# Kernel optimization log

Measured on AMD Instinct MI355X. Metric: run time of the kernel, lower is better.

Reference implementation:

```python
import jax, jax.numpy as jnp
import numpy as np

# dims: B batch, C features, N nodes, L seq_len, P pred_len, D d_model, M topk+self,
# H hidden(=4D), K date2vec freqs, DM time_features, PPH points_per_hour
B, C, N, L, P, D, M, H, K, DM, PPH = 32, 3, 883, 12, 12, 128, 10, 512, 16, 5, 12


def setup_inputs() -> dict:
    ks = jax.random.split(jax.random.key(0), 24)
    r = lambda i, shape, s=1.0: jax.random.normal(ks[i], shape, dtype=jnp.float32) * s
    z = lambda shape: jnp.zeros(shape, jnp.float32)
    return {
        "input": r(0, (B, C, N, L)),
        "adj": r(1, (N, N)),
        "seqs_time": jax.random.uniform(ks[2], (B, DM, 1, L), dtype=jnp.float32) - 0.5,
        "targets_time": jax.random.uniform(ks[3], (B, DM, 1, P), dtype=jnp.float32) - 0.5,
        "memory_bank": r(4, (N, D), (2.0 / (N + D)) ** 0.5),
        "We1": r(5, (D, D), D ** -0.5),
        "We2": r(6, (D, D), D ** -0.5),
        "time_in_day_emb": r(7, (PPH * 24, D), 0.05),
        "day_in_week_emb": r(8, (7, D), 0.05),
        "ts_emb_W": r(9, (D, C * L), (C * L) ** -0.5),
        "ts_emb_b": z((D,)),
        "conv_in_W": r(10, (C, C), C ** -0.5),
        "conv_in_b": z((C,)),
        "enc_W1": r(11, (3, H, H), H ** -0.5),
        "enc_b1": z((3, H)),
        "enc_W2": r(12, (3, H, H), H ** -0.5),
        "enc_b2": z((3, H)),
        "reg_W": r(13, (C * L, H), H ** -0.5),
        "reg_b": z((C * L,)),
        "d2v_w0": r(14, (DM,), 0.1),
        "d2v_b0": r(15, (1,), 0.1),
        "d2v_W": r(16, (K, DM), 0.3),
        "d2v_b": r(17, (K,), 0.3),
        "d2v_mix": r(18, (1,), 0.1),
        "weight_inextend": r(19, (M,), 0.3),
        "fus_W": r(20, (C, D), C ** -0.5),
        "fus_b": z((D,)),
        "glu_W1": r(21, (D, C), D ** -0.5),
        "glu_b1": z((C,)),
        "glu_W2": r(22, (D, C), D ** -0.5),
        "glu_b2": z((C,)),
    }


def _forward(input, adj, seqs_time, targets_time, memory_bank, We1, We2,
             time_in_day_emb, day_in_week_emb, ts_emb_W, ts_emb_b,
             conv_in_W, conv_in_b, enc_W1, enc_b1, enc_W2, enc_b2,
             reg_W, reg_b, d2v_w0, d2v_b0, d2v_W, d2v_b, d2v_mix,
             weight_inextend, fus_W, fus_b, glu_W1, glu_b1, glu_W2, glu_b2):
    eps = 1e-5

    def bn(x):  # train-mode BatchNorm2d, identity affine (default init)
        m = x.mean((0, 2, 3), keepdims=True)
        v = x.var((0, 2, 3), keepdims=True)
        return (x - m) * jax.lax.rsqrt(v + eps)

    # --- adaptive adjacency: matmul + row standardize + masked softmax ---
    e1 = memory_bank @ We1
    e2 = memory_bank @ We2
    a = e1 @ e2.T  # [N, N]
    a = (a - a.mean(-1, keepdims=True)) / jnp.std(a, axis=-1, ddof=1, keepdims=True)
    a = jax.nn.softmax(jax.nn.relu(a) - jnp.eye(N, dtype=a.dtype) * 1e6, axis=-1)

    xb = bn(input)  # [B, C, N, L]

    # --- Input module (STID-style) ---
    ts = xb.transpose(0, 2, 1, 3).reshape(B, N, C * L)  # [B, N, C*L]
    ts_emb = jnp.einsum('bnk,dk->bdn', ts, ts_emb_W) + ts_emb_b[None, :, None]
    hour = (seqs_time[:, -2, 0, :] + 0.5) * 23.0
    minute = (seqs_time[:, -1, 0, :] + 0.5) * 59.0
    tidx = jnp.clip(((hour * 60.0 + minute) / (60.0 / PPH))[:, -1].astype(jnp.int32), 0, PPH * 24 - 1)
    didx = jnp.clip(((seqs_time[:, 2, 0, -1] + 0.5) * 6.0).astype(jnp.int32), 0, 6)
    tid = jnp.broadcast_to(time_in_day_emb[tidx][:, :, None], (B, D, N))
    diw = jnp.broadcast_to(day_in_week_emb[didx][:, :, None], (B, D, N))
    node = jnp.broadcast_to(memory_bank.T[None], (B, D, N))
    hidden = jnp.concatenate([ts_emb, node, tid, diw], axis=1)  # [B, 4D, N]
    for i in range(3):  # MLP residual blocks (1x1 conv == channel matmul)
        h = jax.nn.relu(jnp.einsum('hk,bkn->bhn', enc_W1[i], hidden) + enc_b1[i][None, :, None])
        hidden = hidden + jnp.einsum('hk,bkn->bhn', enc_W2[i], h) + enc_b2[i][None, :, None]
    reg = jnp.einsum('ok,bkn->bon', reg_W, hidden) + reg_b[None, :, None]  # [B, C*L, N]
    hid = bn(reg.reshape(B, C, L, N).transpose(0, 1, 3, 2))  # [B, C, N, L]
    cx = jnp.einsum('oc,bcnl->bonl', conv_in_W, xb) + conv_in_b[None, :, None, None]
    x = bn(hid + cx)

    # --- sample module: topk neighbors + gather ---
    top_value, index = jax.lax.top_k(a, M - 1)  # [N, M-1]
    x_ext = jnp.concatenate([x[:, :, :, None, :], x[:, :, index]], axis=3)  # [B,C,N,M,L]

    # --- Date2Vec (Time2Vec-style periodic embedding) ---
    tau = jnp.concatenate([seqs_time, targets_time], axis=-1)[:, :, 0, :]  # [B, DM, L+P]
    phi = (jnp.einsum('bdt,d->bt', tau, d2v_w0) + d2v_b0[0]
           + jnp.sin(jnp.einsum('bdt,kd->bkt', tau, d2v_W) + d2v_b[None, :, None]).sum(1))
    d2v = phi[:, None, None, None, :] + d2v_mix[0] * x_ext.mean(-1)[..., None]  # [B,C,N,M,L+P]
    d2v_x, d2v_y = d2v[..., :L], d2v[..., L:]

    # --- Fusion: date-attention over source timesteps, neighbor-weighted merge ---
    scores = jnp.einsum('bcnmp,bcnml->bnmpl', d2v_y, d2v_x) / jnp.float32(C * L)
    A = jax.nn.softmax(scores, axis=-1)
    pm = jnp.einsum('bnmpl,bcnml->bcnmp', A, x_ext)
    w = jnp.concatenate([jnp.ones((N, 1), pm.dtype), top_value], axis=-1) * weight_inextend[None, :]
    pred = jnp.einsum('bcnmp,nm->bcnp', pm, w)
    pred = jnp.einsum('bcnp,cd->bdnp', pred, fus_W) + fus_b[None, :, None, None]

    # --- GLU output module ---
    o1 = jnp.einsum('bdnp,do->bonp', pred, glu_W1) + glu_b1[None, :, None, None]
    o2 = jnp.einsum('bdnp,do->bonp', pred, glu_W2) + glu_b2[None, :, None, None]
    return o1 * jax.nn.sigmoid(o2)  # [B, C, N, P]


def reference(input, adj, seqs_time, targets_time, memory_bank, We1, We2,
              time_in_day_emb, day_in_week_emb, ts_emb_W, ts_emb_b,
              conv_in_W, conv_in_b, enc_W1, enc_b1, enc_W2, enc_b2,
              reg_W, reg_b, d2v_w0, d2v_b0, d2v_W, d2v_b, d2v_mix,
              weight_inextend, fus_W, fus_b, glu_W1, glu_b1, glu_W2, glu_b2):
    return _forward(input, adj, seqs_time, targets_time, memory_bank, We1, We2,
                    time_in_day_emb, day_in_week_emb, ts_emb_W, ts_emb_b,
                    conv_in_W, conv_in_b, enc_W1, enc_b1, enc_W2, enc_b2,
                    reg_W, reg_b, d2v_w0, d2v_b0, d2v_W, d2v_b, d2v_mix,
                    weight_inextend, fus_W, fus_b, glu_W1, glu_b1, glu_W2, glu_b2)
```

## Files before the change

### kernel.cpp

```cpp
#include <hip/hip_runtime.h>
#include <hip/hip_bf16.h>


#define NN 883
#define NPAD 896
#define BB 32
#define HH 512
#define NL 10596
#define CNT_PER_C 339072.0f
#define TOT_X 1017216
#define LSTR 32
#define LREG 4096

typedef __attribute__((ext_vector_type(8))) short bf16x8;
typedef __attribute__((ext_vector_type(4))) float f32x4;

static __device__ __forceinline__ float bf2f(__hip_bfloat16 v) { return __bfloat162float(v); }
static __device__ __forceinline__ float ldf(const void* p, long i, int f) {
    return f ? ((const float*)p)[i] : bf2f(((const __hip_bfloat16*)p)[i]);
}
static __device__ __forceinline__ unsigned short bfbits(float v) {
    __hip_bfloat16 h = __float2bfloat16(v);
    return *(unsigned short*)&h;
}
static __device__ __forceinline__ void async_copy16(const void* g, void* l) {
    __builtin_amdgcn_global_load_lds((const __attribute__((address_space(1))) void*)g,
                                     (__attribute__((address_space(3))) void*)l, 16, 0, 0);
}

struct alignas(8) BF4 { __hip_bfloat16 a, b, c, d; };

__global__ void k_sent_r10(float* __restrict__ out, int n)
{
    int i = blockIdx.x*256 + threadIdx.x;
    if (i < n) out[i] = 1000.0f;
}

__global__ void k_probe_r10(const unsigned short* __restrict__ u, int* __restrict__ flag)
{
    int t = threadIdx.x, cnt = 0;
    for (int i = t; i < 4096; i += 256) {
        int e = (u[i] >> 7) & 0xFF;
        cnt += (e >= 0xC0);
    }
    __shared__ int r[256];
    r[t] = cnt; __syncthreads();
    for (int s = 128; s > 0; s >>= 1) { if (t < s) r[t] += r[t+s]; __syncthreads(); }
    if (t == 0) *flag = (r[0] > 8) ? 1 : 0;
}

__global__ void k_wsplit_r10(const void* __restrict__ src, const int* __restrict__ dflag,
                             int n, __hip_bfloat16* __restrict__ hi,
                             __hip_bfloat16* __restrict__ lo)
{
    int f = *dflag;
    for (int i = blockIdx.x*256 + threadIdx.x; i < n; i += gridDim.x*256) {
        float v = ldf(src, i, f);
        __hip_bfloat16 h = __float2bfloat16(v);
        hi[i] = h;
        lo[i] = __float2bfloat16(v - bf2f(h));
    }
}

__global__ void k_prep_r10(const void* __restrict__ seqs, const void* __restrict__ tgts,
                           const void* __restrict__ w0, const void* __restrict__ b0,
                           const void* __restrict__ d2vW, const void* __restrict__ d2vb,
                           const void* __restrict__ fusW, const void* __restrict__ fusb,
                           const void* __restrict__ g1W, const void* __restrict__ g1b,
                           const void* __restrict__ g2W, const void* __restrict__ g2b,
                           const int* __restrict__ dflag,
                           int* __restrict__ tidx, int* __restrict__ didx,
                           float* __restrict__ phi, float* __restrict__ wc)
{
    int f = *dflag, t = threadIdx.x;
    if (t < 32) {
        int b = t;
        float h  = (ldf(seqs, (b*5+3)*12 + 11, f) + 0.5f) * 23.0f;
        float mi = (ldf(seqs, (b*5+4)*12 + 11, f) + 0.5f) * 59.0f;
        int ti = (int)((h * 60.0f + mi) / 5.0f);
        tidx[b] = ti < 0 ? 0 : (ti > 287 ? 287 : ti);
        int di = (int)((ldf(seqs, (b*5+2)*12 + 11, f) + 0.5f) * 6.0f);
        didx[b] = di < 0 ? 0 : (di > 6 ? 6 : di);
    }
    for (int i = t; i < 768; i += 256) {
        int b = i / 24, tt = i % 24;
        float tau[5];
        #pragma unroll
        for (int d = 0; d < 5; d++)
            tau[d] = (tt < 12) ? ldf(seqs, (b*5+d)*12 + tt, f)
                               : ldf(tgts, (b*5+d)*12 + tt - 12, f);
        float s = ldf(b0, 0, f);
        #pragma unroll
        for (int d = 0; d < 5; d++) s += tau[d] * ldf(w0, d, f);
        for (int k = 0; k < 16; k++) {
            float arg = ldf(d2vb, k, f);
            #pragma unroll
            for (int d = 0; d < 5; d++) arg += tau[d] * ldf(d2vW, k*5 + d, f);
            s += sinf(arg);
        }
        phi[i] = s;
    }
    if (t < 24) {
        if (t < 9) {
            int o = t / 3, c = t % 3; float s = 0.f;
            for (int d = 0; d < 128; d++) s += ldf(fusW, c*128+d, f) * ldf(g1W, d*3+o, f);
            wc[t] = s;
        } else if (t < 12) {
            int o = t - 9; float s = ldf(g1b, o, f);
            for (int d = 0; d < 128; d++) s += ldf(fusb, d, f) * ldf(g1W, d*3+o, f);
            wc[9 + o] = s;
        } else if (t < 21) {
            int j = t - 12; int o = j / 3, c = j % 3; float s = 0.f;
            for (int d = 0; d < 128; d++) s += ldf(fusW, c*128+d, f) * ldf(g2W, d*3+o, f);
            wc[12 + j] = s;
        } else {
            int o = t - 21; float s = ldf(g2b, o, f);
            for (int d = 0; d < 128; d++) s += ldf(fusb, d, f) * ldf(g2W, d*3+o, f);
            wc[21 + o] = s;
        }
    }
}

__global__ void k_e_r10(const void* __restrict__ mb, const void* __restrict__ We1,
                        const void* __restrict__ We2, const int* __restrict__ dflag,
                        float* __restrict__ e1, float* __restrict__ e2t)
{
    int f = *dflag;
    int idx = blockIdx.x*256 + threadIdx.x;
    int which = idx >= 113024;
    int j = which ? idx - 113024 : idx;
    int d = j & 127, n = j >> 7;
    const void* W = which ? We2 : We1;
    float s = 0.f;
    for (int k = 0; k < 128; k++)
        s += ldf(mb, n*128 + k, f) * ldf(W, k*128 + d, f);
    if (which) e2t[d*NN + n] = s;
    else       e1[j] = s;
}

__global__ void __launch_bounds__(256)
k_graph_r10(const float* __restrict__ e1, const float* __restrict__ e2t,
            float* __restrict__ topval, int* __restrict__ topidx)
{
    int n = blockIdx.x, t = threadIdx.x;
    __shared__ float e1s[128];
    __shared__ float arow[NN];
    __shared__ float red[256];
    __shared__ int redi[256];
    if (t < 128) e1s[t] = e1[n*128 + t];
    __syncthreads();
    for (int m = t; m < NN; m += 256) {
        float acc = 0.f;
        #pragma unroll 8
        for (int k = 0; k < 128; k++) acc += e1s[k] * e2t[k*NN + m];
        arow[m] = acc;
    }
    __syncthreads();
    float s = 0.f;
    for (int m = t; m < NN; m += 256) s += arow[m];
    red[t] = s; __syncthreads();
    for (int st = 128; st > 0; st >>= 1) { if (t < st) red[t] += red[t+st]; __syncthreads(); }
    float mean = red[0] / 883.0f; __syncthreads();
    float ss = 0.f;
    for (int m = t; m < NN; m += 256) { float d = arow[m] - mean; ss += d*d; }
    red[t] = ss; __syncthreads();
    for (int st = 128; st > 0; st >>= 1) { if (t < st) red[t] += red[t+st]; __syncthreads(); }
    float rstd = 1.0f / sqrtf(red[0] / 882.0f); __syncthreads();
    for (int m = t; m < NN; m += 256) {
        float z = (arow[m] - mean) * rstd;
        z = fmaxf(z, 0.f);
        if (m == n) z -= 1e6f;
        arow[m] = z;
    }
    __syncthreads();
    float mx = -3.4e38f;
    for (int m = t; m < NN; m += 256) mx = fmaxf(mx, arow[m]);
    red[t] = mx; __syncthreads();
    for (int st = 128; st > 0; st >>= 1) { if (t < st) red[t] = fmaxf(red[t], red[t+st]); __syncthreads(); }
    float M = red[0]; __syncthreads();
    float ds = 0.f;
    for (int m = t; m < NN; m += 256) { float e = expf(arow[m] - M); arow[m] = e; ds += e; }
    red[t] = ds; __syncthreads();
    for (int st = 128; st > 0; st >>= 1) { if (t < st) red[t] += red[t+st]; __syncthreads(); }
    float inv = 1.0f / red[0]; __syncthreads();
    for (int m = t; m < NN; m += 256) arow[m] *= inv;
    __syncthreads();
    for (int j = 0; j < 9; j++) {
        float bv = -1.f; int bi = 0;
        for (int m = t; m < NN; m += 256) { float v = arow[m]; if (v > bv) { bv = v; bi = m; } }
        red[t] = bv; redi[t] = bi; __syncthreads();
        for (int st = 128; st > 0; st >>= 1) {
            if (t < st) {
                float ov = red[t+st]; int oi = redi[t+st];
                if (ov > red[t] || (ov == red[t] && oi < redi[t])) { red[t] = ov; redi[t] = oi; }
            }
            __syncthreads();
        }
        if (t == 0) {
            topval[n*9 + j] = red[0];
            topidx[n*9 + j] = redi[0];
            arow[redi[0]] = -1.f;
        }
        __syncthreads();
    }
}

__global__ void k_bn1_r10(const void* __restrict__ x, const int* __restrict__ dflag,
                          float* __restrict__ st)
{
    int f = *dflag;
    float s[3] = {0,0,0}, q[3] = {0,0,0};
    for (int i = blockIdx.x*256 + threadIdx.x; i < TOT_X; i += 512*256) {
        int c = (i / NL) % 3;
        float v = ldf(x, i, f);
        s[c] += v; q[c] += v*v;
    }
    __shared__ float red[6][256];
    int t = threadIdx.x;
    #pragma unroll
    for (int j = 0; j < 3; j++) { red[j][t] = s[j]; red[3+j][t] = q[j]; }
    __syncthreads();
    for (int st_ = 128; st_ > 0; st_ >>= 1) {
        if (t < st_) {
            #pragma unroll
            for (int j = 0; j < 6; j++) red[j][t] += red[j][t+st_];
        }
        __syncthreads();
    }
    if (t < 6) atomicAdd(&st[t], red[t][0]);
}

__global__ void __launch_bounds__(256)
k_hid_r10(const void* __restrict__ in, const void* __restrict__ mb,
          const void* __restrict__ tide, const void* __restrict__ diwe,
          const void* __restrict__ tsW, const void* __restrict__ tsb,
          const int* __restrict__ tidx, const int* __restrict__ didx,
          const int* __restrict__ dflag, const float* __restrict__ st1,
          int b0, __hip_bfloat16* __restrict__ Xhi, __hip_bfloat16* __restrict__ Xlo)
{
    int f = *dflag;
    int n = blockIdx.x, bl = blockIdx.y, bg = b0 + bl, t = threadIdx.x;
    __shared__ float tsw[128*37];
    __shared__ float tsbs[128];
    __shared__ float xbs[36];
    for (int i = t; i < 4608; i += 256) {
        int ch = i / 36, k = i % 36;
        tsw[ch*37 + k] = ldf(tsW, i, f);
    }
    if (t < 128) tsbs[t] = ldf(tsb, t, f);
    if (t < 36) {
        int c = t / 12, l = t % 12;
        float m = st1[c] * (1.0f/CNT_PER_C);
        float v = st1[3+c] * (1.0f/CNT_PER_C) - m*m;
        xbs[t] = (ldf(in, ((long)(bg*3 + c)*NN + n)*12 + l, f) - m) / sqrtf(v + 1e-5f);
    }
    __syncthreads();
    size_t base = ((size_t)bl*NPAD + n)*HH;
    float v[2];
    #pragma unroll
    for (int j = 0; j < 2; j++) {
        int ch = 2*t + j;
        if (ch < 128) {
            float a = tsbs[ch];
            #pragma unroll
            for (int k = 0; k < 36; k++) a += xbs[k] * tsw[ch*37 + k];
            v[j] = a;
        } else if (ch < 256) v[j] = ldf(mb, n*128 + ch - 128, f);
        else if (ch < 384)   v[j] = ldf(tide, tidx[bg]*128 + ch - 256, f);
        else                 v[j] = ldf(diwe, didx[bg]*128 + ch - 384, f);
    }
    unsigned short h0 = bfbits(v[0]), h1 = bfbits(v[1]);
    __hip_bfloat16 hb0, hb1;
    *(unsigned short*)&hb0 = h0; *(unsigned short*)&hb1 = h1;
    unsigned short l0 = bfbits(v[0] - bf2f(hb0)), l1 = bfbits(v[1] - bf2f(hb1));
    *(unsigned*)(Xhi + base + 2*t) = (unsigned)h0 | ((unsigned)h1 << 16);
    *(unsigned*)(Xlo + base + 2*t) = (unsigned)l0 | ((unsigned)l1 << 16);
}

template<bool RELU, bool RESID, bool F32OUT>
__global__ void __launch_bounds__(256)
k_gemm_r10(const __hip_bfloat16* __restrict__ Whi, const __hip_bfloat16* __restrict__ Wlo,
           long Woff, const void* __restrict__ bias, long boff,
           const int* __restrict__ dflag,
           const __hip_bfloat16* __restrict__ Xhi, const __hip_bfloat16* __restrict__ Xlo,
           __hip_bfloat16* __restrict__ Yhi, __hip_bfloat16* __restrict__ Ylo,
           float* __restrict__ outF, int HO, int b0)
{
    __shared__ __align__(16) short sm[4*LREG];
    int tid = threadIdx.x, bz = blockIdx.z;
    int n0 = blockIdx.x * 128, ho0 = blockIdx.y * 128;
    int lane = tid & 63, wave = tid >> 6;
    int wm = wave & 1, wn = wave >> 1;
    int lm = lane & 15, quad = lane >> 4;

    f32x4 acc[4][4];
    #pragma unroll
    for (int i = 0; i < 4; i++)
        #pragma unroll
        for (int j = 0; j < 4; j++) acc[i][j] = (f32x4){0.f, 0.f, 0.f, 0.f};

    const size_t xb0 = (size_t)bz*NPAD*HH;
    int rowi[2], kci[2], rri[2], nBi[2], lofsi[2];
    #pragma unroll
    for (int it = 0; it < 2; it++) {
        int s = it*256 + tid;
        rowi[it] = s >> 2; kci[it] = (s & 3) * 8;
        int rr = ho0 + rowi[it]; rri[it] = (rr >= HO) ? HO - 1 : rr;
        int nB = n0 + rowi[it]; nBi[it] = (nB >= NN) ? NN - 1 : nB;
        lofsi[it] = s * 8;
    }

    for (int k0 = 0; k0 < 512; k0 += 32) {
        #pragma unroll
        for (int it = 0; it < 2; it++) {
            size_t wofs = (size_t)Woff + (size_t)rri[it]*512 + k0 + kci[it];
            size_t xofs = xb0 + (size_t)nBi[it]*HH + k0 + kci[it];
            int lofs = lofsi[it];
            async_copy16(Whi + wofs, &sm[lofs]);
            async_copy16(Wlo + wofs, &sm[LREG + lofs]);
            async_copy16(Xhi + xofs, &sm[2*LREG + lofs]);
            async_copy16(Xlo + xofs, &sm[3*LREG + lofs]);
        }
        __syncthreads();
        bf16x8 ah[4], al[4], bh[4], bl[4];
        #pragma unroll
        for (int mi = 0; mi < 4; mi++) {
            int o = (wm*64 + mi*16 + lm)*LSTR + quad*8;
            ah[mi] = *(const bf16x8*)&sm[o];
            al[mi] = *(const bf16x8*)&sm[LREG + o];
        }
        #pragma unroll
        for (int ni = 0; ni < 4; ni++) {
            int o = (wn*64 + ni*16 + lm)*LSTR + quad*8;
            bh[ni] = *(const bf16x8*)&sm[2*LREG + o];
            bl[ni] = *(const bf16x8*)&sm[3*LREG + o];
        }
        #pragma unroll
        for (int mi = 0; mi < 4; mi++)
            #pragma unroll
            for (int ni = 0; ni < 4; ni++) {
                acc[mi][ni] = __builtin_amdgcn_mfma_f32_16x16x32_bf16(ah[mi], bh[ni], acc[mi][ni], 0, 0, 0);
                acc[mi][ni] = __builtin_amdgcn_mfma_f32_16x16x32_bf16(ah[mi], bl[ni], acc[mi][ni], 0, 0, 0);
                acc[mi][ni] = __builtin_amdgcn_mfma_f32_16x16x32_bf16(al[mi], bh[ni], acc[mi][ni], 0, 0, 0);
            }
        __syncthreads();
    }

    int f = *dflag;
    #pragma unroll
    for (int mi = 0; mi < 4; mi++) {
        int hor = ho0 + wm*64 + mi*16 + quad*4;
        float bv[4];
        #pragma unroll
        for (int r = 0; r < 4; r++) {
            int h = hor + r; if (h >= HO) h = HO - 1;
            bv[r] = ldf(bias, boff + h, f);
        }
        #pragma unroll
        for (int ni = 0; ni < 4; ni++) {
            int nc = n0 + wn*64 + ni*16 + lm;
            if (nc >= NN) continue;
            if constexpr (F32OUT) {
                #pragma unroll
                for (int r = 0; r < 4; r++) {
                    int h = hor + r;
                    if (h < HO) outF[((size_t)(b0 + bz)*HO + h)*NN + nc] = acc[mi][ni][r] + bv[r];
                }
            } else {
                size_t o = xb0 + (size_t)nc*HH + hor;
                float vals[4];
                #pragma unroll
                for (int r = 0; r < 4; r++) vals[r] = acc[mi][ni][r] + bv[r];
                if constexpr (RESID) {
                    BF4 rh = *(const BF4*)(Yhi + o);
                    BF4 rl = *(const BF4*)(Ylo + o);
                    vals[0] += bf2f(rh.a) + bf2f(rl.a);
                    vals[1] += bf2f(rh.b) + bf2f(rl.b);
                    vals[2] += bf2f(rh.c) + bf2f(rl.c);
                    vals[3] += bf2f(rh.d) + bf2f(rl.d);
                }
                if constexpr (RELU) {
                    #pragma unroll
                    for (int r = 0; r < 4; r++) vals[r] = fmaxf(vals[r], 0.f);
                }
                BF4 hi, lo;
                hi.a = __float2bfloat16(vals[0]); lo.a = __float2bfloat16(vals[0] - bf2f(hi.a));
                hi.b = __float2bfloat16(vals[1]); lo.b = __float2bfloat16(vals[1] - bf2f(hi.b));
                hi.c = __float2bfloat16(vals[2]); lo.c = __float2bfloat16(vals[2] - bf2f(hi.c));
                hi.d = __float2bfloat16(vals[3]); lo.d = __float2bfloat16(vals[3] - bf2f(hi.d));
                *(BF4*)(Yhi + o) = hi;
                *(BF4*)(Ylo + o) = lo;
            }
        }
    }
}

__global__ void k_bn2_r10(const float* __restrict__ x, float* __restrict__ st)
{
    float s[3] = {0,0,0}, q[3] = {0,0,0};
    for (int i = blockIdx.x*256 + threadIdx.x; i < TOT_X; i += 512*256) {
        int c = ((i / NN) % 36) / 12;
        float v = x[i];
        s[c] += v; q[c] += v*v;
    }
    __shared__ float red[6][256];
    int t = threadIdx.x;
    #pragma unroll
    for (int j = 0; j < 3; j++) { red[j][t] = s[j]; red[3+j][t] = q[j]; }
    __syncthreads();
    for (int st_ = 128; st_ > 0; st_ >>= 1) {
        if (t < st_) {
            #pragma unroll
            for (int j = 0; j < 6; j++) red[j][t] += red[j][t+st_];
        }
        __syncthreads();
    }
    if (t < 6) atomicAdd(&st[t], red[t][0]);
}

__global__ void k_xpre_r10(const float* __restrict__ regb, const void* __restrict__ in,
                           const void* __restrict__ convW, const void* __restrict__ convb,
                           const int* __restrict__ dflag, const float* __restrict__ st1,
                           const float* __restrict__ st2, float* __restrict__ st3,
                           float* __restrict__ xpre)
{
    int f = *dflag;
    int i = blockIdx.x*256 + threadIdx.x;
    float s[3] = {0,0,0}, q[3] = {0,0,0};
    if (i < TOT_X) {
        int b = i / 31788, r1 = i % 31788;
        int c = r1 / NL, r2 = r1 % NL;
        int n = r2 / 12, l = r2 % 12;
        float m2 = st2[c] * (1.0f/CNT_PER_C);
        float v2 = st2[3+c] * (1.0f/CNT_PER_C) - m2*m2;
        float hidv = (regb[((size_t)b*36 + c*12 + l)*NN + n] - m2) / sqrtf(v2 + 1e-5f);
        float cx = ldf(convb, c, f);
        #pragma unroll
        for (int cc = 0; cc < 3; cc++) {
            float m1 = st1[cc] * (1.0f/CNT_PER_C);
            float v1 = st1[3+cc] * (1.0f/CNT_PER_C) - m1*m1;
            float xbv = (ldf(in, ((long)(b*3 + cc)*NN + n)*12 + l, f) - m1) / sqrtf(v1 + 1e-5f);
            cx += ldf(convW, c*3 + cc, f) * xbv;
        }
        float v = hidv + cx;
        xpre[i] = v;
        s[c] = v; q[c] = v*v;
    }
    __shared__ float red[6][256];
    int t = threadIdx.x;
    #pragma unroll
    for (int j = 0; j < 3; j++) { red[j][t] = s[j]; red[3+j][t] = q[j]; }
    __syncthreads();
    for (int st_ = 128; st_ > 0; st_ >>= 1) {
        if (t < st_) {
            #pragma unroll
            for (int j = 0; j < 6; j++) red[j][t] += red[j][t+st_];
        }
        __syncthreads();
    }
    if (t < 6) atomicAdd(&st3[t], red[t][0]);
}

__global__ void __launch_bounds__(64)
k_tail_r10(const float* __restrict__ xpre, const float* __restrict__ st3,
           const float* __restrict__ phi, const float* __restrict__ topval,
           const int* __restrict__ topidx, const float* __restrict__ wc,
           const void* __restrict__ wie, const void* __restrict__ mixp,
           const int* __restrict__ dflag, float* __restrict__ out)
{
    int f = *dflag;
    int n = blockIdx.x, b = blockIdx.y, t = threadIdx.x;
    __shared__ float xe[3][10][12], mn[3][10], phis[24], ws[10];
    __shared__ float pm[3][10][12], pred[3][12];
    float m3[3], rs3[3];
    #pragma unroll
    for (int c = 0; c < 3; c++) {
        float m = st3[c] * (1.0f/CNT_PER_C);
        float v = st3[3+c] * (1.0f/CNT_PER_C) - m*m;
        m3[c] = m; rs3[c] = 1.0f / sqrtf(v + 1e-5f);
    }
    if (t < 24) phis[t] = phi[b*24 + t];
    if (t < 10) ws[t] = (t == 0 ? 1.0f : topval[n*9 + t - 1]) * ldf(wie, t, f);
    for (int i = t; i < 360; i += 64) {
        int c = i / 120, m = (i / 12) % 10, l = i % 12;
        int nn2 = (m == 0) ? n : topidx[n*9 + m - 1];
        xe[c][m][l] = (xpre[((size_t)(b*3 + c)*NN + nn2)*12 + l] - m3[c]) * rs3[c];
    }
    __syncthreads();
    if (t < 30) {
        int c = t / 10, m = t % 10;
        float s = 0.f;
        #pragma unroll
        for (int l = 0; l < 12; l++) s += xe[c][m][l];
        mn[c][m] = s * (1.0f/12.0f);
    }
    __syncthreads();
    float mix = ldf(mixp, 0, f);
    for (int pr = t; pr < 120; pr += 64) {
        int m = pr / 12, p = pr % 12;
        float y[3], sc[12], mx = -3.4e38f;
        #pragma unroll
        for (int c = 0; c < 3; c++) y[c] = phis[12+p] + mix*mn[c][m];
        #pragma unroll
        for (int l = 0; l < 12; l++) {
            float v = 0.f;
            #pragma unroll
            for (int c = 0; c < 3; c++) v += y[c] * (phis[l] + mix*mn[c][m]);
            sc[l] = v * (1.0f/36.0f); mx = fmaxf(mx, sc[l]);
        }
        float den = 0.f;
        #pragma unroll
        for (int l = 0; l < 12; l++) { float e = expf(sc[l] - mx); sc[l] = e; den += e; }
        float inv = 1.0f/den;
        float p0 = 0.f, p1 = 0.f, p2 = 0.f;
        #pragma unroll
        for (int l = 0; l < 12; l++) {
            float a = sc[l]*inv;
            p0 += a*xe[0][m][l]; p1 += a*xe[1][m][l]; p2 += a*xe[2][m][l];
        }
        pm[0][m][p] = p0; pm[1][m][p] = p1; pm[2][m][p] = p2;
    }
    __syncthreads();
    if (t < 36) {
        int c = t/12, p = t%12;
        float s = 0.f;
        #pragma unroll
        for (int m = 0; m < 10; m++) s += pm[c][m][p]*ws[m];
        pred[c][p] = s;
    }
    __syncthreads();
    if (t < 36) {
        int o = t/12, p = t%12;
        float o1 = wc[9+o]  + wc[o*3+0]*pred[0][p] + wc[o*3+1]*pred[1][p] + wc[o*3+2]*pred[2][p];
        float o2 = wc[21+o] + wc[12+o*3+0]*pred[0][p] + wc[12+o*3+1]*pred[1][p] + wc[12+o*3+2]*pred[2][p];
        out[((size_t)(b*3 + o)*NN + n)*12 + p] = o1 / (1.0f + expf(-o2));
    }
}

extern "C" void kernel_launch(void* const* d_in, const int* in_sizes, int n_in,
                              void* d_out, int out_size, void* d_ws, size_t ws_size,
                              hipStream_t stream)
{
    (void)in_sizes; (void)n_in;
    char* w = (char*)d_ws;
    auto alloc = [&](size_t bytes) { char* p = w; w += (bytes + 255) & ~(size_t)255; return p; };

    float* regb   = (float*)alloc((size_t)TOT_X*4);
    float* xpre   = (float*)alloc((size_t)TOT_X*4);
    __hip_bfloat16* Whi1 = (__hip_bfloat16*)alloc(786432*2);
    __hip_bfloat16* Wlo1 = (__hip_bfloat16*)alloc(786432*2);
    __hip_bfloat16* Whi2 = (__hip_bfloat16*)alloc(786432*2);
    __hip_bfloat16* Wlo2 = (__hip_bfloat16*)alloc(786432*2);
    __hip_bfloat16* rhi  = (__hip_bfloat16*)alloc(18432*2);
    __hip_bfloat16* rlo  = (__hip_bfloat16*)alloc(18432*2);
    float* e1     = (float*)alloc(113024*4);
    float* e2t    = (float*)alloc(113024*4);
    float* phi    = (float*)alloc(768*4);
    float* topval = (float*)alloc(7947*4);
    int*   topidx = (int*)alloc(7947*4);
    int*   tidx   = (int*)alloc(32*4);
    int*   didx   = (int*)alloc(32*4);
    float* stats  = (float*)alloc(18*4);
    float* wc     = (float*)alloc(24*4);
    int*   dflag  = (int*)alloc(4);
    size_t fixedEnd = (size_t)(w - (char*)d_ws);

    const size_t XB = (size_t)NPAD*HH*2;
    int CH = 0;
    for (int c = 32; c >= 1; c >>= 1) {
        if (fixedEnd + 4*(size_t)c*XB + 4096 <= ws_size) { CH = c; break; }
    }
    if (CH == 0) {
        k_sent_r10<<<(out_size + 255)/256, 256, 0, stream>>>((float*)d_out, out_size);
        return;
    }
    char* regionB = w;
    __hip_bfloat16* Xahi = (__hip_bfloat16*)regionB;
    __hip_bfloat16* Xalo = (__hip_bfloat16*)(regionB + (size_t)CH*XB);
    __hip_bfloat16* Xbhi = (__hip_bfloat16*)(regionB + 2*(size_t)CH*XB);
    __hip_bfloat16* Xblo = (__hip_bfloat16*)(regionB + 3*(size_t)CH*XB);

    hipMemsetAsync(stats, 0, 18*4, stream);

    k_probe_r10<<<1, 256, 0, stream>>>((const unsigned short*)d_in[0], dflag);
    k_prep_r10<<<1, 256, 0, stream>>>(d_in[2], d_in[3], d_in[19], d_in[20], d_in[21], d_in[22],
                                      d_in[25], d_in[26], d_in[27], d_in[28], d_in[29], d_in[30],
                                      dflag, tidx, didx, phi, wc);
    k_wsplit_r10<<<1024, 256, 0, stream>>>(d_in[13], dflag, 786432, Whi1, Wlo1);
    k_wsplit_r10<<<1024, 256, 0, stream>>>(d_in[15], dflag, 786432, Whi2, Wlo2);
    k_wsplit_r10<<<72,   256, 0, stream>>>(d_in[17], dflag, 18432, rhi, rlo);

    k_e_r10<<<883, 256, 0, stream>>>(d_in[4], d_in[5], d_in[6], dflag, e1, e2t);
    k_graph_r10<<<883, 256, 0, stream>>>(e1, e2t, topval, topidx);
    k_bn1_r10<<<512, 256, 0, stream>>>(d_in[0], dflag, stats);

    for (int b0 = 0; b0 < BB; b0 += CH) {
        k_hid_r10<<<dim3(NN, CH), 256, 0, stream>>>(d_in[0], d_in[4], d_in[7], d_in[8],
                                                    d_in[9], d_in[10], tidx, didx, dflag,
                                                    stats, b0, Xahi, Xalo);
        for (int i = 0; i < 3; i++) {
            k_gemm_r10<true, false, false><<<dim3(7, 4, CH), 256, 0, stream>>>(
                Whi1, Wlo1, (long)i*HH*HH, d_in[14], (long)i*HH, dflag,
                Xahi, Xalo, Xbhi, Xblo, (float*)nullptr, HH, b0);
            k_gemm_r10<false, true, false><<<dim3(7, 4, CH), 256, 0, stream>>>(
                Whi2, Wlo2, (long)i*HH*HH, d_in[16], (long)i*HH, dflag,
                Xbhi, Xblo, Xahi, Xalo, (float*)nullptr, HH, b0);
        }
        k_gemm_r10<false, false, true><<<dim3(7, 1, CH), 256, 0, stream>>>(
            rhi, rlo, 0, d_in[18], 0, dflag,
            Xahi, Xalo, (__hip_bfloat16*)nullptr, (__hip_bfloat16*)nullptr, regb, 36, b0);
    }

    k_bn2_r10<<<512, 256, 0, stream>>>(regb, stats + 6);
    k_xpre_r10<<<3974, 256, 0, stream>>>(regb, d_in[0], d_in[11], d_in[12], dflag,
                                         stats, stats + 6, stats + 12, xpre);
    k_tail_r10<<<dim3(NN, BB), 64, 0, stream>>>(xpre, stats + 12, phi, topval, topidx, wc,
                                                d_in[24], d_in[23], dflag, (float*)d_out);
}
```

Before: 975.2 us.

## Fuse second BatchNorm stats into regression GEMM, transpose its output, batch hidden-embedding nodes

New measurement: 918.8 us. 5.8% less time.

```diff
diff --git a/kernel.cpp b/kernel.cpp
--- a/kernel.cpp
+++ b/kernel.cpp
@@ -30,13 +30,13 @@
 
 struct alignas(8) BF4 { __hip_bfloat16 a, b, c, d; };
 
-__global__ void k_sent_r10(float* __restrict__ out, int n)
+__global__ void k_sent_r11(float* __restrict__ out, int n)
 {
     int i = blockIdx.x*256 + threadIdx.x;
     if (i < n) out[i] = 1000.0f;
 }
 
-__global__ void k_probe_r10(const unsigned short* __restrict__ u, int* __restrict__ flag)
+__global__ void k_probe_r11(const unsigned short* __restrict__ u, int* __restrict__ flag)
 {
     int t = threadIdx.x, cnt = 0;
     for (int i = t; i < 4096; i += 256) {
@@ -49,7 +49,7 @@
     if (t == 0) *flag = (r[0] > 8) ? 1 : 0;
 }
 
-__global__ void k_wsplit_r10(const void* __restrict__ src, const int* __restrict__ dflag,
+__global__ void k_wsplit_r11(const void* __restrict__ src, const int* __restrict__ dflag,
                              int n, __hip_bfloat16* __restrict__ hi,
                              __hip_bfloat16* __restrict__ lo)
 {
@@ -62,7 +62,7 @@
     }
 }
 
-__global__ void k_prep_r10(const void* __restrict__ seqs, const void* __restrict__ tgts,
+__global__ void k_prep_r11(const void* __restrict__ seqs, const void* __restrict__ tgts,
                            const void* __restrict__ w0, const void* __restrict__ b0,
                            const void* __restrict__ d2vW, const void* __restrict__ d2vb,
                            const void* __restrict__ fusW, const void* __restrict__ fusb,
@@ -121,7 +121,7 @@
     }
 }
 
-__global__ void k_e_r10(const void* __restrict__ mb, const void* __restrict__ We1,
+__global__ void k_e_r11(const void* __restrict__ mb, const void* __restrict__ We1,
                         const void* __restrict__ We2, const int* __restrict__ dflag,
                         float* __restrict__ e1, float* __restrict__ e2t)
 {
@@ -139,7 +139,7 @@
 }
 
 __global__ void __launch_bounds__(256)
-k_graph_r10(const float* __restrict__ e1, const float* __restrict__ e2t,
+k_graph_r11(const float* __restrict__ e1, const float* __restrict__ e2t,
             float* __restrict__ topval, int* __restrict__ topidx)
 {
     int n = blockIdx.x, t = threadIdx.x;
@@ -205,7 +205,7 @@
     }
 }
 
-__global__ void k_bn1_r10(const void* __restrict__ x, const int* __restrict__ dflag,
+__global__ void k_bn1_r11(const void* __restrict__ x, const int* __restrict__ dflag,
                           float* __restrict__ st)
 {
     int f = *dflag;
@@ -231,7 +231,7 @@
 }
 
 __global__ void __launch_bounds__(256)
-k_hid_r10(const void* __restrict__ in, const void* __restrict__ mb,
+k_hid_r11(const void* __restrict__ in, const void* __restrict__ mb,
           const void* __restrict__ tide, const void* __restrict__ diwe,
           const void* __restrict__ tsW, const void* __restrict__ tsb,
           const int* __restrict__ tidx, const int* __restrict__ didx,
@@ -239,52 +239,73 @@
           int b0, __hip_bfloat16* __restrict__ Xhi, __hip_bfloat16* __restrict__ Xlo)
 {
     int f = *dflag;
-    int n = blockIdx.x, bl = blockIdx.y, bg = b0 + bl, t = threadIdx.x;
+    int bl = blockIdx.y, bg = b0 + bl, t = threadIdx.x;
+    int n0 = blockIdx.x * 8;
     __shared__ float tsw[128*37];
     __shared__ float tsbs[128];
-    __shared__ float xbs[36];
-    for (int i = t; i < 4608; i += 256) {
-        int ch = i / 36, k = i % 36;
-        tsw[ch*37 + k] = ldf(tsW, i, f);
-    }
-    if (t < 128) tsbs[t] = ldf(tsb, t, f);
-    if (t < 36) {
-        int c = t / 12, l = t % 12;
+    __shared__ float xbs[8][36];
+    float m1[3], r1v[3];
+    #pragma unroll
+    for (int c = 0; c < 3; c++) {
         float m = st1[c] * (1.0f/CNT_PER_C);
         float v = st1[3+c] * (1.0f/CNT_PER_C) - m*m;
-        xbs[t] = (ldf(in, ((long)(bg*3 + c)*NN + n)*12 + l, f) - m) / sqrtf(v + 1e-5f);
-    }
-    __syncthreads();
+        m1[c] = m; r1v[c] = 1.0f / sqrtf(v + 1e-5f);
+    }
+    for (int i = t; i < 4608; i += 256)
+        tsw[(i/36)*37 + (i%36)] = ldf(tsW, i, f);
+    if (t < 128) tsbs[t] = ldf(tsb, t, f);
+    for (int i = t; i < 288; i += 256) {
+        int nl = i / 36, k = i % 36;
+        int c = k / 12, l = k % 12;
+        int n = n0 + nl; if (n >= NN) n = NN - 1;
+        xbs[nl][k] = (ldf(in, ((long)(bg*3 + c)*NN + n)*12 + l, f) - m1[c]) * r1v[c];
+    }
+    __syncthreads();
+    int nloc = t >> 5, lane = t & 31;
+    int n = n0 + nloc;
+    if (n >= NN) return;
     size_t base = ((size_t)bl*NPAD + n)*HH;
-    float v[2];
-    #pragma unroll
-    for (int j = 0; j < 2; j++) {
-        int ch = 2*t + j;
-        if (ch < 128) {
-            float a = tsbs[ch];
+    const float* xr = xbs[nloc];
+    #pragma unroll
+    for (int j = 0; j < 8; j++) {
+        int ch0 = j*64 + lane*2;
+        float v0, v1;
+        if (j < 2) {
+            float a0 = tsbs[ch0], a1 = tsbs[ch0+1];
             #pragma unroll
-            for (int k = 0; k < 36; k++) a += xbs[k] * tsw[ch*37 + k];
-            v[j] = a;
-        } else if (ch < 256) v[j] = ldf(mb, n*128 + ch - 128, f);
-        else if (ch < 384)   v[j] = ldf(tide, tidx[bg]*128 + ch - 256, f);
-        else                 v[j] = ldf(diwe, didx[bg]*128 + ch - 384, f);
-    }
-    unsigned short h0 = bfbits(v[0]), h1 = bfbits(v[1]);
-    __hip_bfloat16 hb0, hb1;
-    *(unsigned short*)&hb0 = h0; *(unsigned short*)&hb1 = h1;
-    unsigned short l0 = bfbits(v[0] - bf2f(hb0)), l1 = bfbits(v[1] - bf2f(hb1));
-    *(unsigned*)(Xhi + base + 2*t) = (unsigned)h0 | ((unsigned)h1 << 16);
-    *(unsigned*)(Xlo + base + 2*t) = (unsigned)l0 | ((unsigned)l1 << 16);
-}
-
-template<bool RELU, bool RESID, bool F32OUT>
+            for (int k = 0; k < 36; k++) {
+                float xv = xr[k];
+                a0 += xv * tsw[ch0*37 + k];
+                a1 += xv * tsw[(ch0+1)*37 + k];
+            }
+            v0 = a0; v1 = a1;
+        } else if (j < 4) {
+            v0 = ldf(mb, n*128 + ch0 - 128, f);
+            v1 = ldf(mb, n*128 + ch0 - 127, f);
+        } else if (j < 6) {
+            v0 = ldf(tide, tidx[bg]*128 + ch0 - 256, f);
+            v1 = ldf(tide, tidx[bg]*128 + ch0 - 255, f);
+        } else {
+            v0 = ldf(diwe, didx[bg]*128 + ch0 - 384, f);
+            v1 = ldf(diwe, didx[bg]*128 + ch0 - 383, f);
+        }
+        unsigned short h0 = bfbits(v0), h1 = bfbits(v1);
+        __hip_bfloat16 hb0, hb1;
+        *(unsigned short*)&hb0 = h0; *(unsigned short*)&hb1 = h1;
+        unsigned short l0 = bfbits(v0 - bf2f(hb0)), l1 = bfbits(v1 - bf2f(hb1));
+        *(unsigned*)(Xhi + base + ch0) = (unsigned)h0 | ((unsigned)h1 << 16);
+        *(unsigned*)(Xlo + base + ch0) = (unsigned)l0 | ((unsigned)l1 << 16);
+    }
+}
+
+template<bool RELU, bool RESID, bool REGT>
 __global__ void __launch_bounds__(256)
-k_gemm_r10(const __hip_bfloat16* __restrict__ Whi, const __hip_bfloat16* __restrict__ Wlo,
+k_gemm_r11(const __hip_bfloat16* __restrict__ Whi, const __hip_bfloat16* __restrict__ Wlo,
            long Woff, const void* __restrict__ bias, long boff,
            const int* __restrict__ dflag,
            const __hip_bfloat16* __restrict__ Xhi, const __hip_bfloat16* __restrict__ Xlo,
            __hip_bfloat16* __restrict__ Yhi, __hip_bfloat16* __restrict__ Ylo,
-           float* __restrict__ outF, int HO, int b0)
+           float* __restrict__ regT, float* __restrict__ st2, int HO, int b0)
 {
     __shared__ __align__(16) short sm[4*LREG];
     int tid = threadIdx.x, bz = blockIdx.z;
@@ -300,13 +321,13 @@
         for (int j = 0; j < 4; j++) acc[i][j] = (f32x4){0.f, 0.f, 0.f, 0.f};
 
     const size_t xb0 = (size_t)bz*NPAD*HH;
-    int rowi[2], kci[2], rri[2], nBi[2], lofsi[2];
+    int rri[2], nBi[2], kci[2], lofsi[2];
     #pragma unroll
     for (int it = 0; it < 2; it++) {
         int s = it*256 + tid;
-        rowi[it] = s >> 2; kci[it] = (s & 3) * 8;
-        int rr = ho0 + rowi[it]; rri[it] = (rr >= HO) ? HO - 1 : rr;
-        int nB = n0 + rowi[it]; nBi[it] = (nB >= NN) ? NN - 1 : nB;
+        int row = s >> 2; kci[it] = (s & 3) * 8;
+        int rr = ho0 + row; rri[it] = (rr >= HO) ? HO - 1 : rr;
+        int nB = n0 + row; nBi[it] = (nB >= NN) ? NN - 1 : nB;
         lofsi[it] = s * 8;
     }
 
@@ -347,6 +368,7 @@
     }
 
     int f = *dflag;
+    float s3[3] = {0,0,0}, q3[3] = {0,0,0};
     #pragma unroll
     for (int mi = 0; mi < 4; mi++) {
         int hor = ho0 + wm*64 + mi*16 + quad*4;
@@ -360,11 +382,17 @@
         for (int ni = 0; ni < 4; ni++) {
             int nc = n0 + wn*64 + ni*16 + lm;
             if (nc >= NN) continue;
-            if constexpr (F32OUT) {
-                #pragma unroll
-                for (int r = 0; r < 4; r++) {
-                    int h = hor + r;
-                    if (h < HO) outF[((size_t)(b0 + bz)*HO + h)*NN + nc] = acc[mi][ni][r] + bv[r];
+            if constexpr (REGT) {
+                if (hor <= 32) {
+                    int c = hor / 12;
+                    float4 v4;
+                    v4.x = acc[mi][ni][0] + bv[0];
+                    v4.y = acc[mi][ni][1] + bv[1];
+                    v4.z = acc[mi][ni][2] + bv[2];
+                    v4.w = acc[mi][ni][3] + bv[3];
+                    *(float4*)(regT + ((size_t)(b0 + bz)*NN + nc)*36 + hor) = v4;
+                    s3[c] += v4.x + v4.y + v4.z + v4.w;
+                    q3[c] += v4.x*v4.x + v4.y*v4.y + v4.z*v4.z + v4.w*v4.w;
                 }
             } else {
                 size_t o = xb0 + (size_t)nc*HH + hor;
@@ -393,32 +421,23 @@
             }
         }
     }
-}
-
-__global__ void k_bn2_r10(const float* __restrict__ x, float* __restrict__ st)
-{
-    float s[3] = {0,0,0}, q[3] = {0,0,0};
-    for (int i = blockIdx.x*256 + threadIdx.x; i < TOT_X; i += 512*256) {
-        int c = ((i / NN) % 36) / 12;
-        float v = x[i];
-        s[c] += v; q[c] += v*v;
-    }
-    __shared__ float red[6][256];
-    int t = threadIdx.x;
-    #pragma unroll
-    for (int j = 0; j < 3; j++) { red[j][t] = s[j]; red[3+j][t] = q[j]; }
-    __syncthreads();
-    for (int st_ = 128; st_ > 0; st_ >>= 1) {
-        if (t < st_) {
-            #pragma unroll
-            for (int j = 0; j < 6; j++) red[j][t] += red[j][t+st_];
-        }
+    if constexpr (REGT) {
+        float* red = (float*)sm;
+        #pragma unroll
+        for (int j = 0; j < 3; j++) { red[j*256 + tid] = s3[j]; red[(3+j)*256 + tid] = q3[j]; }
         __syncthreads();
-    }
-    if (t < 6) atomicAdd(&st[t], red[t][0]);
-}
-
-__global__ void k_xpre_r10(const float* __restrict__ regb, const void* __restrict__ in,
+        for (int st = 128; st > 0; st >>= 1) {
+            if (tid < st) {
+                #pragma unroll
+                for (int j = 0; j < 6; j++) red[j*256 + tid] += red[j*256 + tid + st];
+            }
+            __syncthreads();
+        }
+        if (tid < 6) atomicAdd(&st2[tid], red[tid*256]);
+    }
+}
+
+__global__ void k_xpre_r11(const float* __restrict__ regT, const void* __restrict__ in,
                            const void* __restrict__ convW, const void* __restrict__ convb,
                            const int* __restrict__ dflag, const float* __restrict__ st1,
                            const float* __restrict__ st2, float* __restrict__ st3,
@@ -433,7 +452,7 @@
         int n = r2 / 12, l = r2 % 12;
         float m2 = st2[c] * (1.0f/CNT_PER_C);
         float v2 = st2[3+c] * (1.0f/CNT_PER_C) - m2*m2;
-        float hidv = (regb[((size_t)b*36 + c*12 + l)*NN + n] - m2) / sqrtf(v2 + 1e-5f);
+        float hidv = (regT[((size_t)b*NN + n)*36 + c*12 + l] - m2) / sqrtf(v2 + 1e-5f);
         float cx = ldf(convb, c, f);
         #pragma unroll
         for (int cc = 0; cc < 3; cc++) {
@@ -462,7 +481,7 @@
 }
 
 __global__ void __launch_bounds__(64)
-k_tail_r10(const float* __restrict__ xpre, const float* __restrict__ st3,
+k_tail_r11(const float* __restrict__ xpre, const float* __restrict__ st3,
            const float* __restrict__ phi, const float* __restrict__ topval,
            const int* __restrict__ topidx, const float* __restrict__ wc,
            const void* __restrict__ wie, const void* __restrict__ mixp,
@@ -545,7 +564,7 @@
     char* w = (char*)d_ws;
     auto alloc = [&](size_t bytes) { char* p = w; w += (bytes + 255) & ~(size_t)255; return p; };
 
-    float* regb   = (float*)alloc((size_t)TOT_X*4);
+    float* regT   = (float*)alloc((size_t)TOT_X*4);
     float* xpre   = (float*)alloc((size_t)TOT_X*4);
     __hip_bfloat16* Whi1 = (__hip_bfloat16*)alloc(786432*2);
     __hip_bfloat16* Wlo1 = (__hip_bfloat16*)alloc(786432*2);
@@ -571,7 +590,7 @@
         if (fixedEnd + 4*(size_t)c*XB + 4096 <= ws_size) { CH = c; break; }
     }
     if (CH == 0) {
-        k_sent_r10<<<(out_size + 255)/256, 256, 0, stream>>>((float*)d_out, out_size);
+        k_sent_r11<<<(out_size + 255)/256, 256, 0, stream>>>((float*)d_out, out_size);
         return;
     }
     char* regionB = w;
@@ -582,38 +601,38 @@
 
     hipMemsetAsync(stats, 0, 18*4, stream);
 
-    k_probe_r10<<<1, 256, 0, stream>>>((const unsigned short*)d_in[0], dflag);
-    k_prep_r10<<<1, 256, 0, stream>>>(d_in[2], d_in[3], d_in[19], d_in[20], d_in[21], d_in[22],
+    k_probe_r11<<<1, 256, 0, stream>>>((const unsigned short*)d_in[0], dflag);
+    k_prep_r11<<<1, 256, 0, stream>>>(d_in[2], d_in[3], d_in[19], d_in[20], d_in[21], d_in[22],
                                       d_in[25], d_in[26], d_in[27], d_in[28], d_in[29], d_in[30],
                                       dflag, tidx, didx, phi, wc);
-    k_wsplit_r10<<<1024, 256, 0, stream>>>(d_in[13], dflag, 786432, Whi1, Wlo1);
-    k_wsplit_r10<<<1024, 256, 0, stream>>>(d_in[15], dflag, 786432, Whi2, Wlo2);
-    k_wsplit_r10<<<72,   256, 0, stream>>>(d_in[17], dflag, 18432, rhi, rlo);
-
-    k_e_r10<<<883, 256, 0, stream>>>(d_in[4], d_in[5], d_in[6], dflag, e1, e2t);
-    k_graph_r10<<<883, 256, 0, stream>>>(e1, e2t, topval, topidx);
-    k_bn1_r10<<<512, 256, 0, stream>>>(d_in[0], dflag, stats);
+    k_wsplit_r11<<<1024, 256, 0, stream>>>(d_in[13], dflag, 786432, Whi1, Wlo1);
+    k_wsplit_r11<<<1024, 256, 0, stream>>>(d_in[15], dflag, 786432, Whi2, Wlo2);
+    k_wsplit_r11<<<72,   256, 0, stream>>>(d_in[17], dflag, 18432, rhi, rlo);
+
+    k_e_r11<<<883, 256, 0, stream>>>(d_in[4], d_in[5], d_in[6], dflag, e1, e2t);
+    k_graph_r11<<<883, 256, 0, stream>>>(e1, e2t, topval, topidx);
+    k_bn1_r11<<<512, 256, 0, stream>>>(d_in[0], dflag, stats);
 
     for (int b0 = 0; b0 < BB; b0 += CH) {
-        k_hid_r10<<<dim3(NN, CH), 256, 0, stream>>>(d_in[0], d_in[4], d_in[7], d_in[8],
-                                                    d_in[9], d_in[10], tidx, didx, dflag,
-                                                    stats, b0, Xahi, Xalo);
+        k_hid_r11<<<dim3(111, CH), 256, 0, stream>>>(d_in[0], d_in[4], d_in[7], d_in[8],
+                                                     d_in[9], d_in[10], tidx, didx, dflag,
+                                                     stats, b0, Xahi, Xalo);
         for (int i = 0; i < 3; i++) {
-            k_gemm_r10<true, false, false><<<dim3(7, 4, CH), 256, 0, stream>>>(
+            k_gemm_r11<true, false, false><<<dim3(7, 4, CH), 256, 0, stream>>>(
                 Whi1, Wlo1, (long)i*HH*HH, d_in[14], (long)i*HH, dflag,
-                Xahi, Xalo, Xbhi, Xblo, (float*)nullptr, HH, b0);
-            k_gemm_r10<false, true, false><<<dim3(7, 4, CH), 256, 0, stream>>>(
+                Xahi, Xalo, Xbhi, Xblo, (float*)nullptr, (float*)nullptr, HH, b0);
+            k_gemm_r11<false, true, false><<<dim3(7, 4, CH), 256, 0, stream>>>(
                 Whi2, Wlo2, (long)i*HH*HH, d_in[16], (long)i*HH, dflag,
-                Xbhi, Xblo, Xahi, Xalo, (float*)nullptr, HH, b0);
-        }
-        k_gemm_r10<false, false, true><<<dim3(7, 1, CH), 256, 0, stream>>>(
+                Xbhi, Xblo, Xahi, Xalo, (float*)nullptr, (float*)nullptr, HH, b0);
+        }
+        k_gemm_r11<false, false, true><<<dim3(7, 1, CH), 256, 0, stream>>>(
             rhi, rlo, 0, d_in[18], 0, dflag,
-            Xahi, Xalo, (__hip_bfloat16*)nullptr, (__hip_bfloat16*)nullptr, regb, 36, b0);
-    }
-
-    k_bn2_r10<<<512, 256, 0, stream>>>(regb, stats + 6);
-    k_xpre_r10<<<3974, 256, 0, stream>>>(regb, d_in[0], d_in[11], d_in[12], dflag,
+            Xahi, Xalo, (__hip_bfloat16*)nullptr, (__hip_bfloat16*)nullptr,
+            regT, stats + 6, 36, b0);
+    }
+
+    k_xpre_r11<<<3974, 256, 0, stream>>>(regT, d_in[0], d_in[11], d_in[12], dflag,
                                          stats, stats + 6, stats + 12, xpre);
-    k_tail_r10<<<dim3(NN, BB), 64, 0, stream>>>(xpre, stats + 12, phi, topval, topidx, wc,
+    k_tail_r11<<<dim3(NN, BB), 64, 0, stream>>>(xpre, stats + 12, phi, topval, topidx, wc,
                                                 d_in[24], d_in[23], dflag, (float*)d_out);
 }
```
